# Kernel tuning notes

Measured on AMD Instinct MI355X. Metric: run time of the kernel, lower is better.

The kernel has to match this reference:

```python
import jax, jax.numpy as jnp
import numpy as np
from jax import lax

N, M, D = 16384, 4096, 256
CHUNK = 64  # chunk over N for the elementwise min to avoid the O(N*M*D) intermediate


def setup_inputs() -> dict:
    key = jax.random.key(0)
    kz, ke = jax.random.split(key)
    z = jax.random.normal(kz, (N, D), dtype=jnp.float32)
    e = jax.random.normal(ke, (M, D), dtype=jnp.float32)
    return {"z": z, "e": e}


def reference(z, e):
    # --- min_loss: mean over codebook entries of min over latents of squared L2 distance ---
    # GEMM trick: ||z-e||^2 = ||z||^2 + ||e||^2 - 2 z.e
    z2 = jnp.sum(z * z, axis=1)           # [N]
    e2 = jnp.sum(e * e, axis=1)           # [M]
    d2 = z2[:, None] + e2[None, :] - 2.0 * (z @ e.T)  # [N, M]
    min_loss = jnp.mean(jnp.min(d2, axis=0))

    # --- wise_min_loss: mean over (M, D) of elementwise min over N of (z_i - e_j)^2 ---
    # scan over chunks of N with a running min to avoid materializing [N, M, D]
    zc = z.reshape(N // CHUNK, CHUNK, D)
    def step(carry, zb):
        d = (zb[:, None, :] - e[None, :, :]) ** 2  # [CHUNK, M, D]
        return jnp.minimum(carry, jnp.min(d, axis=0)), None
    init = jnp.full((M, D), jnp.inf, dtype=z.dtype)
    wise_min, _ = lax.scan(step, init, zc)  # [M, D]
    wise_min_loss = jnp.mean(wise_min)

    return min_loss, wise_min_loss
```

## Files before the change

kernel.cpp:

```cpp
#include <hip/hip_runtime.h>
#include <hip/hip_bf16.h>

#define N_Z 16384
#define M_E 4096
#define DIM 256
#define NB5 1024
#define BMIN (-6.0f)
#define SCALE5 ((float)NB5 / 12.0f)

typedef __bf16 bf16x8 __attribute__((ext_vector_type(8)));
typedef float f32x4 __attribute__((ext_vector_type(4)));

__device__ __forceinline__ unsigned short f2bf(float f) {
  unsigned u = __float_as_uint(f);
  u = (u + 0x7FFFu + ((u >> 16) & 1u)) >> 16;
  return (unsigned short)u;
}

__device__ __forceinline__ void gl2lds16(const void* g, void* s) {
  __builtin_amdgcn_global_load_lds(
      (const __attribute__((address_space(1))) unsigned*)g,
      (__attribute__((address_space(3))) unsigned*)s, 16, 0, 0);
}

__device__ __forceinline__ unsigned fmap(float f) {
  unsigned u = __float_as_uint(f);
  return (u & 0x80000000u) ? ~u : (u | 0x80000000u);
}
__device__ __forceinline__ float funmap(unsigned u) {
  return __uint_as_float((u & 0x80000000u) ? (u ^ 0x80000000u) : ~u);
}
__device__ __forceinline__ int bucket5(float v) {
  int b = (int)((v - BMIN) * SCALE5);
  return min(max(b, 0), NB5 - 1);
}

__global__ void init_kernel(unsigned* __restrict__ d2min, float* __restrict__ wise_part,
                            float* __restrict__ z2, float* __restrict__ e2) {
  int i = blockIdx.x * blockDim.x + threadIdx.x;
  if (i < M_E) d2min[i] = 0x7F800000u;
  if (i < 64) wise_part[i] = 0.0f;
  if (i < N_Z) z2[i] = 0.0f;
  if (i < M_E) e2[i] = 0.0f;
}

__global__ void prep_kernel(const float* __restrict__ in, float* __restrict__ outT,
                            unsigned short* __restrict__ outB, float* __restrict__ rsum, int R) {
  __shared__ float tile[32][33];
  int r0 = blockIdx.x * 32, c0 = blockIdx.y * 32;
  int tx = threadIdx.x, ty = threadIdx.y;
#pragma unroll
  for (int i = 0; i < 4; ++i) {
    int rr = ty + 8 * i;
    float v = in[(size_t)(r0 + rr) * DIM + c0 + tx];
    tile[rr][tx] = v;
    outB[(size_t)(r0 + rr) * DIM + c0 + tx] = f2bf(v);
    float s = v * v;
#pragma unroll
    for (int o = 1; o < 32; o <<= 1) s += __shfl_xor(s, o);
    if (tx == 0) atomicAdd(&rsum[r0 + rr], s);
  }
  __syncthreads();
#pragma unroll
  for (int i = 0; i < 4; ++i)
    outT[(size_t)(c0 + ty + 8 * i) * R + r0 + tx] = tile[tx][ty + 8 * i];
}

__global__ __launch_bounds__(256, 2) void gemm_min_kernel(
    const unsigned short* __restrict__ zb, const unsigned short* __restrict__ eb,
    const float* __restrict__ z2, const float* __restrict__ e2,
    unsigned* __restrict__ d2min) {
  __shared__ __align__(16) unsigned short lA[128 * 64];
  __shared__ __align__(16) unsigned short lB[128 * 64];

  const int t = threadIdx.x;
  const int w = t >> 6;
  const int l = t & 63;
  const int wr = w >> 1, wc = w & 1;
  int flat = blockIdx.y * 32 + blockIdx.x;
  int nf = (flat >> 3) + (flat & 7) * 512;
  const int tileM = (nf & 31) * 128;
  const int tileN = (nf >> 5) * 128;
  const int l15 = l & 15;
  const int kgr = l >> 4;

  f32x4 acc[4][4];
#pragma unroll
  for (int i = 0; i < 4; ++i)
#pragma unroll
    for (int j = 0; j < 4; ++j) acc[i][j] = (f32x4){0.f, 0.f, 0.f, 0.f};

#pragma unroll 1
  for (int k0 = 0; k0 < DIM; k0 += 64) {
#pragma unroll
    for (int i = 0; i < 4; ++i) {
      int c = i * 256 + t;
      int row = c >> 3;
      int kc = c & 7;
      int kcs = kc ^ (row & 7);
      int ldsbase = (i * 256 + (t & ~63)) * 8;
      gl2lds16(zb + (size_t)(tileN + row) * DIM + (k0 + kcs * 8), &lA[ldsbase]);
      gl2lds16(eb + (size_t)(tileM + row) * DIM + (k0 + kcs * 8), &lB[ldsbase]);
    }
    __syncthreads();

#pragma unroll
    for (int kk = 0; kk < 2; ++kk) {
      bf16x8 a[4], b[4];
      const int kcr = kk * 4 + kgr;
#pragma unroll
      for (int mi = 0; mi < 4; ++mi) {
        int row = wr * 64 + mi * 16 + l15;
        a[mi] = *(const bf16x8*)&lA[row * 64 + ((kcr ^ (row & 7)) * 8)];
      }
#pragma unroll
      for (int ni = 0; ni < 4; ++ni) {
        int row = wc * 64 + ni * 16 + l15;
        b[ni] = *(const bf16x8*)&lB[row * 64 + ((kcr ^ (row & 7)) * 8)];
      }
#pragma unroll
      for (int mi = 0; mi < 4; ++mi)
#pragma unroll
        for (int ni = 0; ni < 4; ++ni)
          acc[mi][ni] = __builtin_amdgcn_mfma_f32_16x16x32_bf16(a[mi], b[ni], acc[mi][ni], 0, 0, 0);
    }
    __syncthreads();
  }

  float* z2s = (float*)lA;
  if (t < 128) z2s[t] = z2[tileN + t];
  __syncthreads();

#pragma unroll
  for (int ni = 0; ni < 4; ++ni) {
    float v = 3.4e38f;
#pragma unroll
    for (int mi = 0; mi < 4; ++mi)
#pragma unroll
      for (int r = 0; r < 4; ++r) {
        int rloc = wr * 64 + mi * 16 + kgr * 4 + r;
        v = fminf(v, z2s[rloc] - 2.0f * acc[mi][ni][r]);
      }
    v = fminf(v, __shfl_xor(v, 16));
    v = fminf(v, __shfl_xor(v, 32));
    if (l < 16) {
      int m = tileM + wc * 64 + ni * 16 + l;
      float d2 = v + e2[m];
      atomicMin(&d2min[m], __float_as_uint(d2));
    }
  }
}

__global__ __launch_bounds__(1024) void wise7_kernel(
    const float* __restrict__ zT, const float* __restrict__ eT,
    float* __restrict__ wise_part) {
  extern __shared__ __align__(16) char smem[];
  float* zs = (float*)smem;
  unsigned* zoff = (unsigned*)(smem + 65536);
  unsigned* pmax = zoff + NB5;
  unsigned* psminN = pmax + NB5;
  __shared__ unsigned scr[16];

  const int d = blockIdx.x, t = threadIdx.x;
  const int lane = t & 63, wid = t >> 6;

  zoff[t] = 0u;
  __syncthreads();

  float zv[16];
  int zbk[16];
  const float4* p = (const float4*)(zT + (size_t)d * N_Z);
#pragma unroll
  for (int i = 0; i < 4; ++i) {
    float4 v = p[i * 1024 + t];
    zv[4 * i + 0] = v.x; zv[4 * i + 1] = v.y; zv[4 * i + 2] = v.z; zv[4 * i + 3] = v.w;
  }
#pragma unroll
  for (int i = 0; i < 16; ++i) {
    zbk[i] = bucket5(zv[i]);
    atomicAdd(&zoff[zbk[i]], 1u);
  }
  __syncthreads();

  {
    unsigned c = zoff[t];
    unsigned incl = c;
#pragma unroll
    for (int o = 1; o < 64; o <<= 1) {
      unsigned v = __shfl_up(incl, o);
      if (lane >= o) incl += v;
    }
    if (lane == 63) scr[wid] = incl;
    __syncthreads();
    if (t == 0) {
      unsigned run = 0;
#pragma unroll
      for (int i = 0; i < 16; ++i) { unsigned v = scr[i]; scr[i] = run; run += v; }
    }
    __syncthreads();
    unsigned excl = scr[wid] + incl - c;
    __syncthreads();
    zoff[t] = excl;
  }
  __syncthreads();

#pragma unroll
  for (int i = 0; i < 16; ++i) {
    unsigned pos = atomicAdd(&zoff[zbk[i]], 1u);
    zs[pos] = zv[i];
  }
  __syncthreads();

  {
    unsigned s0 = t ? zoff[t - 1] : 0u;
    unsigned s1 = zoff[t];
    unsigned mxU = 0u, mnN = 0u;
    for (unsigned j = s0; j < s1; ++j) {
      unsigned u = fmap(zs[j]);
      mxU = max(mxU, u);
      mnN = max(mnN, ~u);
    }
    pmax[t] = mxU;
    psminN[t] = mnN;
  }
  __syncthreads();

  {
    unsigned s = pmax[t];
    unsigned incl = s;
#pragma unroll
    for (int o = 1; o < 64; o <<= 1) {
      unsigned v = __shfl_up(incl, o);
      if (lane >= o) incl = max(incl, v);
    }
    __syncthreads();
    if (lane == 63) scr[wid] = incl;
    __syncthreads();
    if (t == 0) {
      unsigned run = 0;
#pragma unroll
      for (int i = 0; i < 16; ++i) { unsigned v = scr[i]; scr[i] = run; run = max(run, v); }
    }
    __syncthreads();
    pmax[t] = max(scr[wid], incl);
  }
  {
    int tr = NB5 - 1 - t;
    unsigned s = psminN[tr];
    unsigned incl = s;
#pragma unroll
    for (int o = 1; o < 64; o <<= 1) {
      unsigned v = __shfl_up(incl, o);
      if (lane >= o) incl = max(incl, v);
    }
    __syncthreads();
    if (lane == 63) scr[wid] = incl;
    __syncthreads();
    if (t == 0) {
      unsigned run = 0;
#pragma unroll
      for (int i = 0; i < 16; ++i) { unsigned v = scr[i]; scr[i] = run; run = max(run, v); }
    }
    __syncthreads();
    psminN[tr] = max(scr[wid], incl);
  }
  __syncthreads();

  const float* ec = eT + (size_t)d * M_E;
  float accq = 0.0f;
#pragma unroll 1
  for (int q = 0; q < 4; ++q) {
    float ev = ec[q * 1024 + t];
    int b0 = bucket5(ev);
    unsigned s0 = b0 ? zoff[b0 - 1] : 0u;
    unsigned s1 = zoff[b0];
    float best2 = 3.4e38f;
    if (b0 > 0) {
      unsigned u = pmax[b0 - 1];
      if (u) { float dd = funmap(u) - ev; best2 = dd * dd; }
    }
    if (b0 < NB5 - 1) {
      unsigned u = psminN[b0 + 1];
      if (u) { float dd = funmap(~u) - ev; best2 = fminf(best2, dd * dd); }
    }
    for (unsigned j = s0 & ~3u; j < s1; j += 4) {
      float4 zz = *(const float4*)&zs[j];
      float d0 = zz.x - ev, d1 = zz.y - ev;
      float d2 = zz.z - ev, d3 = zz.w - ev;
      best2 = fminf(best2, fminf(fminf(d0 * d0, d1 * d1), fminf(d2 * d2, d3 * d3)));
    }
    accq += best2;
  }

#pragma unroll
  for (int o = 32; o; o >>= 1) accq += __shfl_down(accq, o);
  __syncthreads();
  if (lane == 0) scr[wid] = __float_as_uint(accq);
  __syncthreads();
  if (t == 0) {
    float ssum = 0.0f;
#pragma unroll
    for (int i = 0; i < 16; ++i) ssum += __uint_as_float(scr[i]);
    atomicAdd(&wise_part[d & 63], ssum);
  }
}

__global__ void final_kernel(const unsigned* __restrict__ d2min,
                             const float* __restrict__ wise_part, float* __restrict__ out) {
  __shared__ float red[4];
  int t = threadIdx.x;
  float s = 0.0f;
  for (int m = t; m < M_E; m += 256) s += __uint_as_float(d2min[m]);
#pragma unroll
  for (int off = 32; off; off >>= 1) s += __shfl_down(s, off);
  if ((t & 63) == 0) red[t >> 6] = s;
  __syncthreads();
  if (t == 0) {
    float tot = red[0] + red[1] + red[2] + red[3];
    out[0] = tot / (float)M_E;
    float w = 0.0f;
    for (int i = 0; i < 64; ++i) w += wise_part[i];
    out[1] = w / ((float)M_E * (float)DIM);
  }
}

extern "C" void kernel_launch(void* const* d_in, const int* in_sizes, int n_in,
                              void* d_out, int out_size, void* d_ws, size_t ws_size,
                              hipStream_t stream) {
  const float* z = (const float*)d_in[0];
  const float* e = (const float*)d_in[1];
  float* out = (float*)d_out;

  char* ws = (char*)d_ws;
  unsigned short* zb = (unsigned short*)ws;
  unsigned short* eb = (unsigned short*)(ws + 8388608);
  float* z2 = (float*)(ws + 10485760);
  float* e2 = (float*)(ws + 10551296);
  unsigned* d2min = (unsigned*)(ws + 10567680);
  float* wise_part = (float*)(ws + 10584064);
  float* zT = (float*)(ws + 11534336);
  float* eT = (float*)(ws + 28311552);

  const size_t LDS_WISE = 65536 + 3 * NB5 * 4;
  static int attr_done = 0;
  if (!attr_done) {
    (void)hipFuncSetAttribute((const void*)wise7_kernel,
                              hipFuncAttributeMaxDynamicSharedMemorySize, (int)LDS_WISE);
    attr_done = 1;
  }

  init_kernel<<<64, 256, 0, stream>>>(d2min, wise_part, z2, e2);
  prep_kernel<<<dim3(N_Z / 32, DIM / 32), dim3(32, 8), 0, stream>>>(z, zT, zb, z2, N_Z);
  prep_kernel<<<dim3(M_E / 32, DIM / 32), dim3(32, 8), 0, stream>>>(e, eT, eb, e2, M_E);
  gemm_min_kernel<<<dim3(32, 128), 256, 0, stream>>>(zb, eb, z2, e2, d2min);
  wise7_kernel<<<DIM, 1024, LDS_WISE, stream>>>(zT, eT, wise_part);
  final_kernel<<<1, 256, 0, stream>>>(d2min, wise_part, out);
}
```

Measured before the change: 143.7 us.

## Bucket-sort codebook values per dimension before wise-min search; raise GEMM occupancy

The wise-min kernel now counting-sorts each dimension's 4096 codebook values into buckets in LDS, so neighbouring threads process values from the same or nearby buckets. This reduces divergence in the per-bucket scan loop over sorted z values. The cost is an extra histogram, prefix-scan and scatter pass with several barriers at kernel start. Separately, the GEMM kernel's launch bounds ask for 3 blocks per CU instead of 2, which may force register spilling.

Result: slower. 149.6 us (+4.1%).

```diff
diff --git a/kernel.cpp b/kernel.cpp
--- a/kernel.cpp
+++ b/kernel.cpp
@@ -66,7 +66,7 @@
     outT[(size_t)(c0 + ty + 8 * i) * R + r0 + tx] = tile[tx][ty + 8 * i];
 }
 
-__global__ __launch_bounds__(256, 2) void gemm_min_kernel(
+__global__ __launch_bounds__(256, 3) void gemm_min_kernel(
     const unsigned short* __restrict__ zb, const unsigned short* __restrict__ eb,
     const float* __restrict__ z2, const float* __restrict__ e2,
     unsigned* __restrict__ d2min) {
@@ -151,7 +151,7 @@
   }
 }
 
-__global__ __launch_bounds__(1024) void wise7_kernel(
+__global__ __launch_bounds__(1024) void wise8_kernel(
     const float* __restrict__ zT, const float* __restrict__ eT,
     float* __restrict__ wise_part) {
   extern __shared__ __align__(16) char smem[];
@@ -159,10 +159,56 @@
   unsigned* zoff = (unsigned*)(smem + 65536);
   unsigned* pmax = zoff + NB5;
   unsigned* psminN = pmax + NB5;
+  float* esorted = zs;
+  unsigned* eoff = zoff;
   __shared__ unsigned scr[16];
 
   const int d = blockIdx.x, t = threadIdx.x;
   const int lane = t & 63, wid = t >> 6;
+
+  eoff[t] = 0u;
+  __syncthreads();
+  const float* ec = eT + (size_t)d * M_E;
+  float ev4[4];
+  int ebk[4];
+#pragma unroll
+  for (int i = 0; i < 4; ++i) {
+    ev4[i] = ec[i * 1024 + t];
+    ebk[i] = bucket5(ev4[i]);
+    atomicAdd(&eoff[ebk[i]], 1u);
+  }
+  __syncthreads();
+  {
+    unsigned c = eoff[t];
+    unsigned incl = c;
+#pragma unroll
+    for (int o = 1; o < 64; o <<= 1) {
+      unsigned v = __shfl_up(incl, o);
+      if (lane >= o) incl += v;
+    }
+    if (lane == 63) scr[wid] = incl;
+    __syncthreads();
+    if (t == 0) {
+      unsigned run = 0;
+#pragma unroll
+      for (int i = 0; i < 16; ++i) { unsigned v = scr[i]; scr[i] = run; run += v; }
+    }
+    __syncthreads();
+    unsigned excl = scr[wid] + incl - c;
+    __syncthreads();
+    eoff[t] = excl;
+  }
+  __syncthreads();
+#pragma unroll
+  for (int i = 0; i < 4; ++i) {
+    unsigned pos = atomicAdd(&eoff[ebk[i]], 1u);
+    esorted[pos] = ev4[i];
+  }
+  __syncthreads();
+  float eq[4];
+#pragma unroll
+  for (int q = 0; q < 4; ++q) eq[q] = esorted[q * 1024 + t];
+  __syncthreads();
 
   zoff[t] = 0u;
   __syncthreads();
@@ -266,11 +312,10 @@
   }
   __syncthreads();
 
-  const float* ec = eT + (size_t)d * M_E;
   float accq = 0.0f;
 #pragma unroll 1
   for (int q = 0; q < 4; ++q) {
-    float ev = ec[q * 1024 + t];
+    float ev = eq[q];
     int b0 = bucket5(ev);
     unsigned s0 = b0 ? zoff[b0 - 1] : 0u;
     unsigned s1 = zoff[b0];
@@ -344,7 +389,7 @@
   const size_t LDS_WISE = 65536 + 3 * NB5 * 4;
   static int attr_done = 0;
   if (!attr_done) {
-    (void)hipFuncSetAttribute((const void*)wise7_kernel,
+    (void)hipFuncSetAttribute((const void*)wise8_kernel,
                               hipFuncAttributeMaxDynamicSharedMemorySize, (int)LDS_WISE);
     attr_done = 1;
   }
@@ -353,6 +398,6 @@
   prep_kernel<<<dim3(N_Z / 32, DIM / 32), dim3(32, 8), 0, stream>>>(z, zT, zb, z2, N_Z);
   prep_kernel<<<dim3(M_E / 32, DIM / 32), dim3(32, 8), 0, stream>>>(e, eT, eb, e2, M_E);
   gemm_min_kernel<<<dim3(32, 128), 256, 0, stream>>>(zb, eb, z2, e2, d2min);
-  wise7_kernel<<<DIM, 1024, LDS_WISE, stream>>>(zT, eT, wise_part);
+  wise8_kernel<<<DIM, 1024, LDS_WISE, stream>>>(zT, eT, wise_part);
   final_kernel<<<1, 256, 0, stream>>>(d2min, wise_part, out);
 }
```
